# Kernel tuning notes

Measured on AMD Instinct MI355X. Metric: run time of the kernel, lower is better.

The kernel has to match this reference:

```python
import jax, jax.numpy as jnp
import numpy as np

EPS = 1e-4            # EDM2 normalize() epsilon
NUM_HEADS = 12
ATTN_BALANCE = 0.3
ROPE_BASE = 10000.0
NEG_INF = -1e9


def mp_weight(w):
    """EDM2 MPConv weight: per-output-channel normalize + magnitude-preserving scale.
    w: [out, in] (1x1 conv kernel squeezed)."""
    fan_in = w.shape[1]
    norm = jnp.linalg.norm(w, axis=1, keepdims=True)
    w = w / (EPS + norm * np.float32(np.sqrt(1.0 / fan_in)))  # normalize()
    return w * np.float32(1.0 / np.sqrt(fan_in))              # gain/sqrt(fan_in), gain=1


def apply_rope(q, k):
    """Rotary embedding over the frame index t. q,k: [b, m, t, hw, d]."""
    d = q.shape[-1]
    t = q.shape[2]
    inv_freq = 1.0 / (ROPE_BASE ** (jnp.arange(0, d, 2, dtype=jnp.float32) / d))
    ang = jnp.arange(t, dtype=jnp.float32)[:, None] * inv_freq[None, :]   # [t, d/2]
    cos = jnp.cos(ang)[None, None, :, None, :].astype(q.dtype)
    sin = jnp.sin(ang)[None, None, :, None, :].astype(q.dtype)

    def rot(x):
        x1, x2 = jnp.split(x, 2, axis=-1)
        return jnp.concatenate([x1 * cos - x2 * sin, x1 * sin + x2 * cos], axis=-1)

    return rot(q), rot(k)


def video_attention(x, w_qkv, w_proj, batch_size):
    bt, C, h, w_ = x.shape
    b = batch_size
    t = bt // b
    m = NUM_HEADS
    c = C // m
    hw = h * w_
    S = t * hw

    # MPConv QKV (1x1 conv == channel matmul)
    y = jnp.einsum('oi,bihw->bohw', mp_weight(w_qkv), x)   # [(b t), 3C, h, w]
    # '(b t) (s m c) h w -> s b m t (h w) c'
    y = y.reshape(b, t, 3, m, c, h, w_).transpose(2, 0, 3, 1, 5, 6, 4).reshape(3, b, m, t, hw, c)
    q, k, v = y[0], y[1], y[2]

    q, k = apply_rope(q, k)
    q = q.reshape(b, m, S, c)
    k = k.reshape(b, m, S, c)
    v = v.reshape(b, m, S, c)

    # block-causal video mask: token in frame i attends to all tokens of frames <= i
    frame = jnp.arange(S) // hw
    mask = frame[:, None] >= frame[None, :]                 # [S, S]

    scores = jnp.einsum('bmqc,bmkc->bmqk', q, k) * np.float32(1.0 / np.sqrt(c))
    scores = jnp.where(mask, scores, NEG_INF)
    attn = jax.nn.softmax(scores, axis=-1)
    yo = jnp.einsum('bmqk,bmkc->bmqc', attn, v)             # [b, m, S, c]

    # 'b m (t h w) c -> (b t) (c m) h w'
    yo = yo.reshape(b, m, t, h, w_, c).transpose(0, 2, 5, 1, 3, 4).reshape(bt, C, h, w_)
    yo = jnp.einsum('oi,bihw->bohw', mp_weight(w_proj), yo)

    # mp_sum(x, y, t=attn_balance)
    tb = ATTN_BALANCE
    scale = np.float32(1.0 / np.sqrt((1.0 - tb) ** 2 + tb ** 2))
    return (x * np.float32(1.0 - tb) + yo * np.float32(tb)) * scale


def setup_inputs() -> dict:
    key = jax.random.key(0)
    k1, k2, k3 = jax.random.split(key, 3)
    batch_size = 2
    n_frames = 8
    C, h, w = 768, 16, 16
    x = jax.random.normal(k1, (batch_size * n_frames, C, h, w), dtype=jnp.float32)
    w_qkv = jax.random.normal(k2, (3 * C, C), dtype=jnp.float32)
    w_proj = jax.random.normal(k3, (C, C), dtype=jnp.float32)
    return {"x": x, "w_qkv": w_qkv, "w_proj": w_proj, "batch_size": batch_size}


def reference(x, w_qkv, w_proj, batch_size):
    return video_attention(x, w_qkv, w_proj, batch_size)
```

## Files before the change

kernel.cpp:

```cpp
#include <hip/hip_runtime.h>

typedef __bf16 bf16_t;
typedef __bf16 bf16x4 __attribute__((ext_vector_type(4)));
typedef __bf16 bf16x8 __attribute__((ext_vector_type(8)));
typedef float  f32x4  __attribute__((ext_vector_type(4)));

static constexpr int NHEADS = 12, HC = 64, HW = 256, SEQ = 2048;
static constexpr size_t QKV_ONE = (size_t)2 * NHEADS * SEQ * HC;
static constexpr size_t NSTRIDE = 768 * 256;

__global__ __launch_bounds__(256) void va_prep(const float* __restrict__ wqkv,
                                               const float* __restrict__ wproj,
                                               const float* __restrict__ x,
                                               bf16_t* __restrict__ wout,
                                               bf16_t* __restrict__ xt) {
    int blk = blockIdx.x;
    if (blk < 3072) {
        int row = blk;
        bool is_proj = (row >= 2304);
        const float* wr = is_proj ? wproj + (size_t)(row - 2304) * 768
                                  : wqkv + (size_t)row * 768;
        float part = 0.f;
        for (int i = threadIdx.x; i < 768; i += 256) { float v = wr[i]; part += v * v; }
#pragma unroll
        for (int off = 32; off > 0; off >>= 1) part += __shfl_down(part, off, 64);
        __shared__ float red[4];
        if ((threadIdx.x & 63) == 0) red[threadIdx.x >> 6] = part;
        __syncthreads();
        if (threadIdx.x == 0) {
            float s = red[0] + red[1] + red[2] + red[3];
            red[0] = 1.0f / (2.7712813e-3f + sqrtf(s));
        }
        __syncthreads();
        float sc = red[0];
        for (int i = threadIdx.x; i < 768; i += 256) {
            int j = is_proj ? ((i % 12) * 64 + i / 12) : i;
            wout[(size_t)row * 768 + j] = (bf16_t)(wr[i] * sc);
        }
    } else {
        int t = blk - 3072;
        int n  = t & 15;
        int rest = t >> 4;
        int p0 = (rest & 7) * 32;
        int c0 = (rest >> 3) * 32;
        __shared__ float sm[32][33];
        int tx = threadIdx.x & 31, ty = threadIdx.x >> 5;
        const float* xp = x + (size_t)n * NSTRIDE;
#pragma unroll
        for (int i = 0; i < 4; i++)
            sm[ty + i * 8][tx] = xp[(size_t)(c0 + ty + i * 8) * 256 + p0 + tx];
        __syncthreads();
        bf16_t* xo = xt + (size_t)n * NSTRIDE;
#pragma unroll
        for (int i = 0; i < 4; i++)
            xo[(size_t)(p0 + ty + i * 8) * 768 + c0 + tx] = (bf16_t)sm[tx][ty + i * 8];
    }
}

__global__ __launch_bounds__(256, 2) void va_qkv_mfma(const bf16_t* __restrict__ Wb,
                                                      const bf16_t* __restrict__ xt,
                                                      bf16_t* __restrict__ qkvb) {
    int idx = blockIdx.x;
    int n  = (idx & 7) + 8 * ((idx >> 3) & 1);
    int rest = idx >> 4;
    int p0 = (rest & 1) * 128;
    int m0 = (rest >> 1) * 128;
    int tid = threadIdx.x;
    int lane = tid & 63, w = tid >> 6;
    int lo = lane & 15, hi = lane >> 4;
    int wm = w >> 1, wn = w & 1;
    int lx = lo & 7;

    __shared__ bf16_t Asm[128 * 64];
    __shared__ bf16_t Bsm[128 * 64];

    int srow = tid >> 3, schunk = tid & 7;
    const bf16_t* Ag = Wb + (size_t)(m0 + srow) * 768 + schunk * 8;
    const bf16_t* Bg = xt + (size_t)n * NSTRIDE + (size_t)(p0 + srow) * 768 + schunk * 8;
    int sdst = srow * 128 + ((schunk ^ (srow & 7)) << 4);

    f32x4 acc[4][4];
#pragma unroll
    for (int mt = 0; mt < 4; mt++)
#pragma unroll
        for (int nt = 0; nt < 4; nt++) acc[mt][nt] = (f32x4){0.f, 0.f, 0.f, 0.f};

    bf16x8 sa[4], sb[4];

    auto gload = [&](int k0) {
#pragma unroll
        for (int i = 0; i < 4; i++) {
            sa[i] = *(const bf16x8*)(Ag + (size_t)i * 32 * 768 + k0);
            sb[i] = *(const bf16x8*)(Bg + (size_t)i * 32 * 768 + k0);
        }
    };
    auto swrite = [&]() {
        char* Ac = (char*)Asm;
        char* Bc = (char*)Bsm;
#pragma unroll
        for (int i = 0; i < 4; i++) {
            *(bf16x8*)(Ac + sdst + i * 32 * 128) = sa[i];
            *(bf16x8*)(Bc + sdst + i * 32 * 128) = sb[i];
        }
    };

    gload(0);
    for (int s = 0; s < 12; s++) {
        __syncthreads();
        swrite();
        if (s < 11) gload((s + 1) * 64);
        __syncthreads();
#pragma unroll
        for (int kk = 0; kk < 64; kk += 32) {
            int cb = kk >> 3;
            bf16x8 af[4], bfr[4];
            const char* Ac = (const char*)Asm;
            const char* Bc = (const char*)Bsm;
#pragma unroll
            for (int mt = 0; mt < 4; mt++) {
                int row = wm * 64 + mt * 16 + lo;
                af[mt] = *(const bf16x8*)(Ac + row * 128 + (((cb + hi) ^ lx) << 4));
            }
#pragma unroll
            for (int nt = 0; nt < 4; nt++) {
                int row = wn * 64 + nt * 16 + lo;
                bfr[nt] = *(const bf16x8*)(Bc + row * 128 + (((cb + hi) ^ lx) << 4));
            }
#pragma unroll
            for (int mt = 0; mt < 4; mt++)
#pragma unroll
                for (int nt = 0; nt < 4; nt++)
                    acc[mt][nt] = __builtin_amdgcn_mfma_f32_16x16x32_bf16(af[mt], bfr[nt], acc[mt][nt], 0, 0, 0);
        }
    }

    int head_global = (m0 + wm * 64) >> 6;
    int qkv_idx = head_global / 12;
    int head    = head_global % 12;
    int b = n >> 3, tt = n & 7;
    int bm = b * 12 + head;
    if (qkv_idx < 2) {
        float qsc = (qkv_idx == 0) ? 0.125f : 1.0f;
        float ttf = (float)tt;
#pragma unroll
        for (int mt = 0; mt < 2; mt++)
#pragma unroll
            for (int r = 0; r < 4; r++) {
                int j = mt * 16 + hi * 4 + r;
                float ang = ttf * __expf(-(float)j * 0.2878231366242557f);
                float cs = __cosf(ang), sn = __sinf(ang);
#pragma unroll
                for (int nt = 0; nt < 4; nt++) {
                    float x1 = acc[mt][nt][r], x2 = acc[mt + 2][nt][r];
                    acc[mt][nt][r]     = (x1 * cs - x2 * sn) * qsc;
                    acc[mt + 2][nt][r] = (x1 * sn + x2 * cs) * qsc;
                }
            }
        bf16_t* dst = qkvb + (size_t)qkv_idx * QKV_ONE + ((size_t)bm * SEQ + (size_t)tt * HW) * HC;
#pragma unroll
        for (int mt = 0; mt < 4; mt++)
#pragma unroll
            for (int nt = 0; nt < 4; nt++)
#pragma unroll
                for (int r = 0; r < 4; r++) {
                    int cc = mt * 16 + hi * 4 + r;
                    int p  = p0 + wn * 64 + nt * 16 + lo;
                    dst[(size_t)p * HC + cc] = (bf16_t)acc[mt][nt][r];
                }
    } else {
        bf16_t* dst = qkvb + 2 * QKV_ONE + (size_t)bm * HC * SEQ + (size_t)tt * HW;
#pragma unroll
        for (int mt = 0; mt < 4; mt++)
#pragma unroll
            for (int nt = 0; nt < 4; nt++)
#pragma unroll
                for (int r = 0; r < 4; r++) {
                    int cc = mt * 16 + hi * 4 + r;
                    int p  = p0 + wn * 64 + nt * 16 + lo;
                    dst[(size_t)cc * SEQ + p] = (bf16_t)acc[mt][nt][r];
                }
    }
}

__global__ __launch_bounds__(256, 2) void va_attn(const bf16_t* __restrict__ qkvb,
                                                  bf16_t* __restrict__ yob) {
    int s = blockIdx.x;
    int f = 7 - (s / 96);
    int within = s % 96;
    int bm = within % 24;
    int qs = within / 24;

    int tid = threadIdx.x;
    int w = tid >> 6, lane = tid & 63;
    int lo = lane & 15, hi = lane >> 4;
    int lx = lo & 7;

    const bf16_t* qbase = qkvb + (size_t)bm * SEQ * HC;
    const bf16_t* kbase = qkvb + QKV_ONE + (size_t)bm * SEQ * HC;
    const bf16_t* vbase = qkvb + 2 * QKV_ONE + (size_t)bm * HC * SEQ;

    __shared__ bf16_t PBF[4][64 * 64];
    __shared__ float  Lsm[4][64];
    bf16_t* PBw = PBF[w];

    const bf16_t* qrow = qbase + (size_t)(f * 256 + qs * 64 + lo) * HC;
    bf16x8 qf[4][2];
#pragma unroll
    for (int nq = 0; nq < 4; nq++) {
        qf[nq][0] = *(const bf16x8*)(qrow + (size_t)nq * 16 * HC + hi * 8);
        qf[nq][1] = *(const bf16x8*)(qrow + (size_t)nq * 16 * HC + 32 + hi * 8);
    }
    f32x4 o[4][4];
#pragma unroll
    for (int ct = 0; ct < 4; ct++)
#pragma unroll
        for (int nq = 0; nq < 4; nq++) o[ct][nq] = (f32x4){0.f, 0.f, 0.f, 0.f};
    float l4[4] = {0.f, 0.f, 0.f, 0.f};

    int kend = (f + 1) * 256;

    bf16x8 ka[8];
    {
        const bf16_t* kp = kbase + (size_t)(w * 64 + lo) * HC + hi * 8;
#pragma unroll
        for (int mt = 0; mt < 4; mt++) {
            ka[2 * mt]     = *(const bf16x8*)(kp + (size_t)mt * 16 * HC);
            ka[2 * mt + 1] = *(const bf16x8*)(kp + (size_t)mt * 16 * HC + 32);
        }
    }

    for (int kpos = w * 64; kpos < kend; kpos += 256) {
        const bf16_t* vp = vbase + (size_t)(lo) * SEQ + kpos + hi * 8;
        bf16x8 va[8];
#pragma unroll
        for (int ct = 0; ct < 4; ct++) {
            va[2 * ct]     = *(const bf16x8*)(vp + (size_t)ct * 16 * SEQ);
            va[2 * ct + 1] = *(const bf16x8*)(vp + (size_t)ct * 16 * SEQ + 32);
        }
#pragma unroll
        for (int mt = 0; mt < 4; mt++) {
#pragma unroll
            for (int nq = 0; nq < 4; nq++) {
                f32x4 sacc = (f32x4){0.f, 0.f, 0.f, 0.f};
                sacc = __builtin_amdgcn_mfma_f32_16x16x32_bf16(ka[2 * mt], qf[nq][0], sacc, 0, 0, 0);
                sacc = __builtin_amdgcn_mfma_f32_16x16x32_bf16(ka[2 * mt + 1], qf[nq][1], sacc, 0, 0, 0);
                bf16x4 pk;
#pragma unroll
                for (int r = 0; r < 4; r++) {
                    float p = __expf(sacc[r]);
                    l4[nq] += p;
                    pk[r] = (bf16_t)p;
                }
                *(bf16x4*)(PBw + (nq * 16 + lo) * 64 +
                           (((2 * mt + (hi >> 1)) ^ lx) * 8) + (hi & 1) * 4) = pk;
            }
        }
        int knext = (kpos + 256 < kend) ? kpos + 256 : kpos;
        bf16x8 kan[8];
        {
            const bf16_t* kp = kbase + (size_t)(knext + lo) * HC + hi * 8;
#pragma unroll
            for (int mt = 0; mt < 4; mt++) {
                kan[2 * mt]     = *(const bf16x8*)(kp + (size_t)mt * 16 * HC);
                kan[2 * mt + 1] = *(const bf16x8*)(kp + (size_t)mt * 16 * HC + 32);
            }
        }
        bf16x8 pb0[4], pb1[4];
#pragma unroll
        for (int nq = 0; nq < 4; nq++) {
            pb0[nq] = *(const bf16x8*)(PBw + (nq * 16 + lo) * 64 + (hi ^ lx) * 8);
            pb1[nq] = *(const bf16x8*)(PBw + (nq * 16 + lo) * 64 + ((4 + hi) ^ lx) * 8);
        }
#pragma unroll
        for (int ct = 0; ct < 4; ct++)
#pragma unroll
            for (int nq = 0; nq < 4; nq++) {
                o[ct][nq] = __builtin_amdgcn_mfma_f32_16x16x32_bf16(va[2 * ct], pb0[nq], o[ct][nq], 0, 0, 0);
                o[ct][nq] = __builtin_amdgcn_mfma_f32_16x16x32_bf16(va[2 * ct + 1], pb1[nq], o[ct][nq], 0, 0, 0);
            }
#pragma unroll
        for (int i = 0; i < 8; i++) ka[i] = kan[i];
    }
#pragma unroll
    for (int nq = 0; nq < 4; nq++) {
        l4[nq] += __shfl_xor(l4[nq], 16, 64);
        l4[nq] += __shfl_xor(l4[nq], 32, 64);
    }
    if (hi == 0) {
#pragma unroll
        for (int nq = 0; nq < 4; nq++) Lsm[w][nq * 16 + lo] = l4[nq];
    }
#pragma unroll
    for (int ct = 0; ct < 4; ct++)
#pragma unroll
        for (int nq = 0; nq < 4; nq++) {
            bf16x4 ov;
#pragma unroll
            for (int r = 0; r < 4; r++) ov[r] = (bf16_t)o[ct][nq][r];
            *(bf16x4*)(PBw + (nq * 16 + lo) * 64 +
                       (((2 * ct + (hi >> 1)) ^ lx) * 8) + (hi & 1) * 4) = ov;
        }
    __syncthreads();
    int head = bm % 12, b = bm / 12;
    bf16_t* yb = yob + (size_t)(b * 8 + f) * NSTRIDE + (size_t)(qs * 64) * 768 + head * 64;
#pragma unroll
    for (int i = 0; i < 2; i++) {
        int c = i * 256 + tid;
        int row = c >> 3, j = c & 7;
        int off = row * 64 + ((j ^ (row & 7)) * 8);
        float invl = 1.0f / (Lsm[0][row] + Lsm[1][row] + Lsm[2][row] + Lsm[3][row]);
        bf16x8 p0 = *(const bf16x8*)(PBF[0] + off);
        bf16x8 p1 = *(const bf16x8*)(PBF[1] + off);
        bf16x8 p2 = *(const bf16x8*)(PBF[2] + off);
        bf16x8 p3 = *(const bf16x8*)(PBF[3] + off);
        bf16x8 o8;
#pragma unroll
        for (int r = 0; r < 8; r++)
            o8[r] = (bf16_t)(((float)p0[r] + (float)p1[r] + (float)p2[r] + (float)p3[r]) * invl);
        *(bf16x8*)(yb + (size_t)row * 768 + j * 8) = o8;
    }
}

__global__ __launch_bounds__(256, 2) void va_proj_mfma(const bf16_t* __restrict__ Wb,
                                                       const bf16_t* __restrict__ yob,
                                                       const float* __restrict__ x,
                                                       float* __restrict__ out) {
    int idx = blockIdx.x;
    int n  = (idx & 7) + 8 * ((idx >> 3) & 1);
    int rest = idx >> 4;
    int p0 = (rest & 1) * 128;
    int m0 = (rest >> 1) * 64;
    int tid = threadIdx.x;
    int lane = tid & 63, w = tid >> 6;
    int lo = lane & 15, hi = lane >> 4;

    const bf16_t* Ap = Wb + (size_t)(m0 + lo) * 768 + hi * 8;
    const bf16_t* Bp = yob + (size_t)n * NSTRIDE + (size_t)(p0 + w * 32 + lo) * 768 + hi * 8;

    f32x4 acc[4][2];
#pragma unroll
    for (int mt = 0; mt < 4; mt++)
#pragma unroll
        for (int nt = 0; nt < 2; nt++) acc[mt][nt] = (f32x4){0.f, 0.f, 0.f, 0.f};

    for (int k0 = 0; k0 < 768; k0 += 32) {
        bf16x8 af[4], bfr[2];
#pragma unroll
        for (int mt = 0; mt < 4; mt++)
            af[mt] = *(const bf16x8*)(Ap + (size_t)mt * 16 * 768 + k0);
#pragma unroll
        for (int nt = 0; nt < 2; nt++)
            bfr[nt] = *(const bf16x8*)(Bp + (size_t)nt * 16 * 768 + k0);
#pragma unroll
        for (int mt = 0; mt < 4; mt++)
#pragma unroll
            for (int nt = 0; nt < 2; nt++)
                acc[mt][nt] = __builtin_amdgcn_mfma_f32_16x16x32_bf16(af[mt], bfr[nt], acc[mt][nt], 0, 0, 0);
    }

    const float* xn = x + (size_t)n * NSTRIDE;
    float* on = out + (size_t)n * NSTRIDE;
#pragma unroll
    for (int mt = 0; mt < 4; mt++)
#pragma unroll
        for (int nt = 0; nt < 2; nt++)
#pragma unroll
            for (int r = 0; r < 4; r++) {
                int oo = m0 + mt * 16 + hi * 4 + r;
                int p  = p0 + w * 32 + nt * 16 + lo;
                size_t idx2 = (size_t)oo * 256 + p;
                on[idx2] = (xn[idx2] * 0.7f + acc[mt][nt][r] * 0.3f) * 1.3130643f;
            }
}

extern "C" void kernel_launch(void* const* d_in, const int* in_sizes, int n_in,
                              void* d_out, int out_size, void* d_ws, size_t ws_size,
                              hipStream_t stream) {
    const float* x     = (const float*)d_in[0];
    const float* wqkv  = (const float*)d_in[1];
    const float* wproj = (const float*)d_in[2];
    float* out = (float*)d_out;

    bf16_t* Opart = (bf16_t*)d_ws;
    float*  lpart = (float*)(Opart + (size_t)24 * 36 * 16384);
    bf16_t* wqkv_nb  = (bf16_t*)(lpart + (size_t)24 * 36 * 256);
    bf16_t* xt       = wqkv_nb + (size_t)3072 * 768;
    bf16_t* qkvb     = xt + NSTRIDE * 16;
    bf16_t* yob      = qkvb + 3 * QKV_ONE;

    va_prep<<<6144, 256, 0, stream>>>(wqkv, wproj, x, wqkv_nb, xt);
    va_qkv_mfma<<<576, 256, 0, stream>>>(wqkv_nb, xt, qkvb);
    va_attn<<<768, 256, 0, stream>>>(qkvb, yob);
    va_proj_mfma<<<384, 256, 0, stream>>>(wqkv_nb + (size_t)2304 * 768, yob, x, out);
}
```

Measured before the change: 171.2 us.

## Use raw exp2, split softmax/PV scheduling with setprio, stage proj GEMM in LDS

The Q scale now folds in log2(e), so the attention softmax can use the raw v_exp_f32 (base-2) instruction instead of __expf. The score/exp loop is split in halves, with the P-buffer reads interleaved between them and s_setprio raising wave priority around MFMA sections, so LDS reads overlap with compute. Separately, the projection GEMM now stages A and B tiles through swizzled shared memory with register prefetch, instead of each wave reading global memory directly. The changes add LDS use and barriers to the projection kernel and rely on inline asm for the exponential.

```diff
diff --git a/kernel.cpp b/kernel.cpp
--- a/kernel.cpp
+++ b/kernel.cpp
@@ -140,7 +140,7 @@
     int b = n >> 3, tt = n & 7;
     int bm = b * 12 + head;
     if (qkv_idx < 2) {
-        float qsc = (qkv_idx == 0) ? 0.125f : 1.0f;
+        float qsc = (qkv_idx == 0) ? 0.18033688011f : 1.0f;
         float ttf = (float)tt;
 #pragma unroll
         for (int mt = 0; mt < 2; mt++)
@@ -237,8 +237,9 @@
             va[2 * ct]     = *(const bf16x8*)(vp + (size_t)ct * 16 * SEQ);
             va[2 * ct + 1] = *(const bf16x8*)(vp + (size_t)ct * 16 * SEQ + 32);
         }
-#pragma unroll
-        for (int mt = 0; mt < 4; mt++) {
+        __builtin_amdgcn_s_setprio(1);
+#pragma unroll
+        for (int mt = 0; mt < 2; mt++) {
 #pragma unroll
             for (int nq = 0; nq < 4; nq++) {
                 f32x4 sacc = (f32x4){0.f, 0.f, 0.f, 0.f};
@@ -247,7 +248,8 @@
                 bf16x4 pk;
 #pragma unroll
                 for (int r = 0; r < 4; r++) {
-                    float p = __expf(sacc[r]);
+                    float p;
+                    asm("v_exp_f32 %0, %1" : "=v"(p) : "v"(sacc[r]));
                     l4[nq] += p;
                     pk[r] = (bf16_t)p;
                 }
@@ -255,6 +257,32 @@
                            (((2 * mt + (hi >> 1)) ^ lx) * 8) + (hi & 1) * 4) = pk;
             }
         }
+        __builtin_amdgcn_s_setprio(0);
+        bf16x8 pb0[4], pb1[4];
+#pragma unroll
+        for (int nq = 0; nq < 4; nq++)
+            pb0[nq] = *(const bf16x8*)(PBw + (nq * 16 + lo) * 64 + (hi ^ lx) * 8);
+        __builtin_amdgcn_s_setprio(1);
+#pragma unroll
+        for (int mt = 2; mt < 4; mt++) {
+#pragma unroll
+            for (int nq = 0; nq < 4; nq++) {
+                f32x4 sacc = (f32x4){0.f, 0.f, 0.f, 0.f};
+                sacc = __builtin_amdgcn_mfma_f32_16x16x32_bf16(ka[2 * mt], qf[nq][0], sacc, 0, 0, 0);
+                sacc = __builtin_amdgcn_mfma_f32_16x16x32_bf16(ka[2 * mt + 1], qf[nq][1], sacc, 0, 0, 0);
+                bf16x4 pk;
+#pragma unroll
+                for (int r = 0; r < 4; r++) {
+                    float p;
+                    asm("v_exp_f32 %0, %1" : "=v"(p) : "v"(sacc[r]));
+                    l4[nq] += p;
+                    pk[r] = (bf16_t)p;
+                }
+                *(bf16x4*)(PBw + (nq * 16 + lo) * 64 +
+                           (((2 * mt + (hi >> 1)) ^ lx) * 8) + (hi & 1) * 4) = pk;
+            }
+        }
+        __builtin_amdgcn_s_setprio(0);
         int knext = (kpos + 256 < kend) ? kpos + 256 : kpos;
         bf16x8 kan[8];
         {
@@ -265,19 +293,21 @@
                 kan[2 * mt + 1] = *(const bf16x8*)(kp + (size_t)mt * 16 * HC + 32);
             }
         }
-        bf16x8 pb0[4], pb1[4];
-#pragma unroll
-        for (int nq = 0; nq < 4; nq++) {
-            pb0[nq] = *(const bf16x8*)(PBw + (nq * 16 + lo) * 64 + (hi ^ lx) * 8);
+#pragma unroll
+        for (int nq = 0; nq < 4; nq++)
             pb1[nq] = *(const bf16x8*)(PBw + (nq * 16 + lo) * 64 + ((4 + hi) ^ lx) * 8);
-        }
+        __builtin_amdgcn_s_setprio(1);
 #pragma unroll
         for (int ct = 0; ct < 4; ct++)
 #pragma unroll
-            for (int nq = 0; nq < 4; nq++) {
+            for (int nq = 0; nq < 4; nq++)
                 o[ct][nq] = __builtin_amdgcn_mfma_f32_16x16x32_bf16(va[2 * ct], pb0[nq], o[ct][nq], 0, 0, 0);
+#pragma unroll
+        for (int ct = 0; ct < 4; ct++)
+#pragma unroll
+            for (int nq = 0; nq < 4; nq++)
                 o[ct][nq] = __builtin_amdgcn_mfma_f32_16x16x32_bf16(va[2 * ct + 1], pb1[nq], o[ct][nq], 0, 0, 0);
-            }
+        __builtin_amdgcn_s_setprio(0);
 #pragma unroll
         for (int i = 0; i < 8; i++) ka[i] = kan[i];
     }
@@ -333,9 +363,15 @@
     int tid = threadIdx.x;
     int lane = tid & 63, w = tid >> 6;
     int lo = lane & 15, hi = lane >> 4;
-
-    const bf16_t* Ap = Wb + (size_t)(m0 + lo) * 768 + hi * 8;
-    const bf16_t* Bp = yob + (size_t)n * NSTRIDE + (size_t)(p0 + w * 32 + lo) * 768 + hi * 8;
+    int lx = lo & 7;
+
+    __shared__ bf16_t Asm[64 * 64];
+    __shared__ bf16_t Bsm[128 * 64];
+
+    int srow = tid >> 3, schunk = tid & 7;
+    const bf16_t* Ag = Wb + (size_t)(m0 + srow) * 768 + schunk * 8;
+    const bf16_t* Bg = yob + (size_t)n * NSTRIDE + (size_t)(p0 + srow) * 768 + schunk * 8;
+    int sdst = srow * 128 + ((schunk ^ (srow & 7)) << 4);
 
     f32x4 acc[4][2];
 #pragma unroll
@@ -343,19 +379,54 @@
 #pragma unroll
         for (int nt = 0; nt < 2; nt++) acc[mt][nt] = (f32x4){0.f, 0.f, 0.f, 0.f};
 
-    for (int k0 = 0; k0 < 768; k0 += 32) {
-        bf16x8 af[4], bfr[2];
-#pragma unroll
-        for (int mt = 0; mt < 4; mt++)
-            af[mt] = *(const bf16x8*)(Ap + (size_t)mt * 16 * 768 + k0);
-#pragma unroll
-        for (int nt = 0; nt < 2; nt++)
-            bfr[nt] = *(const bf16x8*)(Bp + (size_t)nt * 16 * 768 + k0);
-#pragma unroll
-        for (int mt = 0; mt < 4; mt++)
-#pragma unroll
-            for (int nt = 0; nt < 2; nt++)
-                acc[mt][nt] = __builtin_amdgcn_mfma_f32_16x16x32_bf16(af[mt], bfr[nt], acc[mt][nt], 0, 0, 0);
+    bf16x8 sa[2], sb[4];
+    auto gload = [&](int k0) {
+#pragma unroll
+        for (int i = 0; i < 2; i++)
+            sa[i] = *(const bf16x8*)(Ag + (size_t)i * 32 * 768 + k0);
+#pragma unroll
+        for (int i = 0; i < 4; i++)
+            sb[i] = *(const bf16x8*)(Bg + (size_t)i * 32 * 768 + k0);
+    };
+    auto swrite = [&]() {
+        char* Ac = (char*)Asm;
+        char* Bc = (char*)Bsm;
+#pragma unroll
+        for (int i = 0; i < 2; i++)
+            *(bf16x8*)(Ac + sdst + i * 32 * 128) = sa[i];
+#pragma unroll
+        for (int i = 0; i < 4; i++)
+            *(bf16x8*)(Bc + sdst + i * 32 * 128) = sb[i];
+    };
+
+    gload(0);
+    for (int s = 0; s < 12; s++) {
+        __syncthreads();
+        swrite();
+        if (s < 11) gload((s + 1) * 64);
+        __syncthreads();
+#pragma unroll
+        for (int kk = 0; kk < 64; kk += 32) {
+            int cb = kk >> 3;
+            bf16x8 af[4], bfr[2];
+            const char* Ac = (const char*)Asm;
+            const char* Bc = (const char*)Bsm;
+#pragma unroll
+            for (int mt = 0; mt < 4; mt++) {
+                int row = mt * 16 + lo;
+                af[mt] = *(const bf16x8*)(Ac + row * 128 + (((cb + hi) ^ lx) << 4));
+            }
+#pragma unroll
+            for (int nt = 0; nt < 2; nt++) {
+                int row = w * 32 + nt * 16 + lo;
+                bfr[nt] = *(const bf16x8*)(Bc + row * 128 + (((cb + hi) ^ lx) << 4));
+            }
+#pragma unroll
+            for (int mt = 0; mt < 4; mt++)
+#pragma unroll
+                for (int nt = 0; nt < 2; nt++)
+                    acc[mt][nt] = __builtin_amdgcn_mfma_f32_16x16x32_bf16(af[mt], bfr[nt], acc[mt][nt], 0, 0, 0);
+        }
     }
 
     const float* xn = x + (size_t)n * NSTRIDE;
```

New measurement: 151.2 us (median of 2 runs). 1.13x faster.
